# Optimization experiments

Hardware: AMD Instinct MI355X
Metric: run time of the kernel (lower is better)

## Reference

```python
import jax, jax.numpy as jnp
import numpy as np
from jax import lax

EPS = 1e-12  # torch F.normalize eps

def setup_inputs() -> dict:
    key = jax.random.key(0)
    k1, k2, k3, k4, k5 = jax.random.split(key, 5)
    N = 4194304
    L = 64
    return {
        "T": jax.random.normal(k1, (1,), dtype=jnp.float32),
        "closed_manifold": jax.random.normal(k2, (N, 2), dtype=jnp.float32),
        "Ws": jax.random.normal(k3, (L, 2, 2), dtype=jnp.float32) * 0.5,
        "bs": jax.random.normal(k4, (L, 2), dtype=jnp.float32) * 0.1,
        "final_W": jax.random.normal(k5, (2, 2), dtype=jnp.float32) * 0.5,
    }

def reference(T, closed_manifold, Ws, bs, final_W):
    # T is accepted but unused, exactly as in the original forward.
    def step(X, wb):
        W, b = wb                      # W: [2,2], b: [2]
        Y = X @ W.T + b                # linear: [N,2]
        A = jnp.tanh(Y)                # activation
        X = (A + Y) * 0.5              # residual averaging (skip_connections=True)
        return X, None
    X, _ = lax.scan(step, closed_manifold, (Ws, bs))
    X = X @ final_W.T                  # final bias-free linear
    # F.normalize(X, p=2, dim=1): row-wise unit vectors with eps clamp
    norm = jnp.sqrt(jnp.sum(X * X, axis=-1, keepdims=True))
    X = X / jnp.maximum(norm, EPS)
    return X
```

## Files before the change

kernel.cpp:

```cpp
#include <hip/hip_runtime.h>


#define KPT 8
#define BLOCK 256

__global__ __launch_bounds__(BLOCK) void nig_kernel(
    const float* __restrict__ X_in,
    const float* __restrict__ Ws,
    const float* __restrict__ bs,
    const float* __restrict__ fW,
    float* __restrict__ out,
    int M,
    int L)
{
    const int tid = blockIdx.x * blockDim.x + threadIdx.x;
    const int nthreads = gridDim.x * blockDim.x;
    const float4* __restrict__ in4 = (const float4*)X_in;
    float4* __restrict__ out4 = (float4*)out;

    const float C     = 2.8853900817779268f;
    const float halfC = 1.4426950408889634f;

    float u0[KPT], u1[KPT];
    int idx[KPT / 2]; bool ok[KPT / 2];
    #pragma unroll
    for (int j = 0; j < KPT / 2; ++j) {
        idx[j] = tid + j * nthreads;
        ok[j] = idx[j] < M;
        float4 v = ok[j] ? in4[idx[j]] : make_float4(0.f, 0.f, 0.f, 0.f);
        u0[2 * j]     = v.x * C; u1[2 * j]     = v.y * C;
        u0[2 * j + 1] = v.z * C; u1[2 * j + 1] = v.w * C;
    }

    float4 w = ((const float4*)Ws)[0];
    float2 b = ((const float2*)bs)[0];

    #pragma unroll 2
    for (int l = 0; l < L; ++l) {
        const int ln = (l + 1 < L) ? (l + 1) : l;
        float4 wn = ((const float4*)Ws)[ln];
        float2 bn = ((const float2*)bs)[ln];

        const float cb0 = C * b.x;
        const float cb1 = C * b.y;
        #pragma unroll
        for (int k = 0; k < KPT; ++k) {
            float y0 = fmaf(w.x, u0[k], fmaf(w.y, u1[k], cb0));
            float y1 = fmaf(w.z, u0[k], fmaf(w.w, u1[k], cb1));
            float e0 = __builtin_amdgcn_exp2f(y0);
            float e1 = __builtin_amdgcn_exp2f(y1);
            float r0 = __builtin_amdgcn_rcpf(e0 + 1.0f);
            float r1 = __builtin_amdgcn_rcpf(e1 + 1.0f);
            u0[k] = fmaf(-C, r0, fmaf(0.5f, y0, halfC));
            u1[k] = fmaf(-C, r1, fmaf(0.5f, y1, halfC));
        }
        w = wn; b = bn;
    }

    const float g0 = fW[0], g1 = fW[1], g2 = fW[2], g3 = fW[3];

    #pragma unroll
    for (int j = 0; j < KPT / 2; ++j) {
        if (!ok[j]) continue;
        float4 o;
        #pragma unroll
        for (int h = 0; h < 2; ++h) {
            const int k = 2 * j + h;
            float z0 = fmaf(g0, u0[k], g1 * u1[k]);
            float z1 = fmaf(g2, u0[k], g3 * u1[k]);
            float s  = fmaf(z0, z0, z1 * z1);
            float n  = __builtin_amdgcn_sqrtf(s);
            float iv = __builtin_amdgcn_rcpf(fmaxf(n, 1e-12f));
            if (h == 0) { o.x = z0 * iv; o.y = z1 * iv; }
            else        { o.z = z0 * iv; o.w = z1 * iv; }
        }
        out4[idx[j]] = o;
    }
}

extern "C" void kernel_launch(void* const* d_in, const int* in_sizes, int n_in,
                              void* d_out, int out_size, void* d_ws, size_t ws_size,
                              hipStream_t stream) {
    const float* X  = (const float*)d_in[1];
    const float* Ws = (const float*)d_in[2];
    const float* bs = (const float*)d_in[3];
    const float* fW = (const float*)d_in[4];
    float* out = (float*)d_out;

    const int L = in_sizes[2] / 4;
    const int M = in_sizes[1] / 4;
    const int threads = (M + (KPT / 2) - 1) / (KPT / 2);
    const int grid = (threads + BLOCK - 1) / BLOCK;

    nig_kernel<<<grid, BLOCK, 0, stream>>>(X, Ws, bs, fW, out, M, L);
}
```

Baseline: 190.5 us.

## Batch eight reciprocals into one with a product tree and clamp exponents

Replaces the per-element reciprocal in the tanh computation with a batched-inverse trick. For each group of 4 points, the 8 denominators are multiplied together, a single rcp is taken, and the individual inverses are recovered with multiplies. This trades 7 transcendental-unit rcps for about 20 extra VALU multiplies. Exponent inputs are clamped so the product of up to 8 terms cannot overflow float, and the launch bounds now request 4 blocks per CU while the outer-loop unroll pragma is removed.

```diff
diff --git a/kernel.cpp b/kernel.cpp
--- a/kernel.cpp
+++ b/kernel.cpp
@@ -4,7 +4,7 @@
 #define KPT 8
 #define BLOCK 256
 
-__global__ __launch_bounds__(BLOCK) void nig_kernel(
+__global__ __launch_bounds__(BLOCK, 4) void nig_kernel(
     const float* __restrict__ X_in,
     const float* __restrict__ Ws,
     const float* __restrict__ bs,
@@ -20,6 +20,7 @@
 
     const float C     = 2.8853900817779268f;
     const float halfC = 1.4426950408889634f;
+    const float YCLMP = 13.3f;
 
     float u0[KPT], u1[KPT];
     int idx[KPT / 2]; bool ok[KPT / 2];
@@ -35,7 +36,6 @@
     float4 w = ((const float4*)Ws)[0];
     float2 b = ((const float2*)bs)[0];
 
-    #pragma unroll 2
     for (int l = 0; l < L; ++l) {
         const int ln = (l + 1 < L) ? (l + 1) : l;
         float4 wn = ((const float4*)Ws)[ln];
@@ -43,16 +43,42 @@
 
         const float cb0 = C * b.x;
         const float cb1 = C * b.y;
+
         #pragma unroll
-        for (int k = 0; k < KPT; ++k) {
-            float y0 = fmaf(w.x, u0[k], fmaf(w.y, u1[k], cb0));
-            float y1 = fmaf(w.z, u0[k], fmaf(w.w, u1[k], cb1));
-            float e0 = __builtin_amdgcn_exp2f(y0);
-            float e1 = __builtin_amdgcn_exp2f(y1);
-            float r0 = __builtin_amdgcn_rcpf(e0 + 1.0f);
-            float r1 = __builtin_amdgcn_rcpf(e1 + 1.0f);
-            u0[k] = fmaf(-C, r0, fmaf(0.5f, y0, halfC));
-            u1[k] = fmaf(-C, r1, fmaf(0.5f, y1, halfC));
+        for (int g = 0; g < KPT / 4; ++g) {
+            float y0[4], y1[4], d0[4], d1[4];
+            #pragma unroll
+            for (int p = 0; p < 4; ++p) {
+                const int k = g * 4 + p;
+                y0[p] = fmaf(w.x, u0[k], fmaf(w.y, u1[k], cb0));
+                y1[p] = fmaf(w.z, u0[k], fmaf(w.w, u1[k], cb1));
+                d0[p] = __builtin_amdgcn_exp2f(fminf(y0[p], YCLMP)) + 1.0f;
+                d1[p] = __builtin_amdgcn_exp2f(fminf(y1[p], YCLMP)) + 1.0f;
+            }
+            float pA = d0[0] * d1[0];
+            float pB = d0[1] * d1[1];
+            float pC = d0[2] * d1[2];
+            float pD = d0[3] * d1[3];
+            float qAB = pA * pB, qCD = pC * pD;
+            float R = __builtin_amdgcn_rcpf(qAB * qCD);
+            float iAB = R * qCD;
+            float iCD = R * qAB;
+            float iA = iAB * pB;
+            float iB = iAB * pA;
+            float iC = iCD * pD;
+            float iD = iCD * pC;
+            float r00 = iA * d1[0], r10 = iA * d0[0];
+            float r01 = iB * d1[1], r11 = iB * d0[1];
+            float r02 = iC * d1[2], r12 = iC * d0[2];
+            float r03 = iD * d1[3], r13 = iD * d0[3];
+            u0[g * 4 + 0] = fmaf(-C, r00, fmaf(0.5f, y0[0], halfC));
+            u1[g * 4 + 0] = fmaf(-C, r10, fmaf(0.5f, y1[0], halfC));
+            u0[g * 4 + 1] = fmaf(-C, r01, fmaf(0.5f, y0[1], halfC));
+            u1[g * 4 + 1] = fmaf(-C, r11, fmaf(0.5f, y1[1], halfC));
+            u0[g * 4 + 2] = fmaf(-C, r02, fmaf(0.5f, y0[2], halfC));
+            u1[g * 4 + 2] = fmaf(-C, r12, fmaf(0.5f, y1[2], halfC));
+            u0[g * 4 + 3] = fmaf(-C, r03, fmaf(0.5f, y0[3], halfC));
+            u1[g * 4 + 3] = fmaf(-C, r13, fmaf(0.5f, y1[3], halfC));
         }
         w = wn; b = bn;
     }
```

After: 212.6 us. 1.12x slower.
